# Kernel optimization log

Measured on AMD Instinct MI355X. Metric: run time of the kernel, lower is better.

Reference implementation:

```python
import jax, jax.numpy as jnp
import numpy as np

N, K, F = 65536, 32, 128


def setup_inputs() -> dict:
    key = jax.random.key(0)
    k1, k2, k3, k4 = jax.random.split(key, 4)
    x = jax.random.normal(k1, (N, F), dtype=jnp.float32)
    means = jax.random.normal(k2, (K, F), dtype=jnp.float32)
    # lower-triangular Cholesky factors of precisions with strictly positive diagonal
    a = jax.random.normal(k3, (K, F, F), dtype=jnp.float32) * 0.05
    precisions_chol = jnp.tril(a, k=-1) + jnp.eye(F, dtype=jnp.float32)[None] * (
        1.0 + 0.1 * jax.random.uniform(k3, (K, 1, 1), dtype=jnp.float32)
    )
    # valid mixture weights on the simplex (log is taken in forward)
    u = jax.random.uniform(k4, (K,), dtype=jnp.float32) + 0.1
    weights = u / jnp.sum(u)
    return {"x": x, "means": means, "precisions_chol": precisions_chol, "weights": weights}


def reference(x, means, precisions_chol, weights):
    n_features = x.shape[1]
    # log|prec_chol_k| = sum of log diagonal entries  -> [K]
    log_det = jnp.sum(jnp.log(jnp.diagonal(precisions_chol, axis1=1, axis2=2)), axis=1)
    # whitened residuals: (x - mu_k) @ P_k  done as two batched GEMMs -> [N,K,F]
    y = jnp.einsum("nf,kfg->nkg", x, precisions_chol) - jnp.einsum(
        "kf,kfg->kg", means, precisions_chol
    )[None, :, :]
    log_prob = jnp.sum(y * y, axis=-1)  # Mahalanobis^2, [N,K]
    log2pi = jnp.log(jnp.asarray(2.0 * np.pi, dtype=x.dtype))
    log_gauss = -0.5 * (n_features * log2pi + log_prob) + log_det[None, :]
    # NLL-ish score: logsumexp over components with log mixture weights -> [N]
    return jax.nn.logsumexp(log_gauss + jnp.log(weights)[None, :], axis=1)
```

## Files before the change

### kernel.cpp

```cpp
#include <hip/hip_runtime.h>
#include <hip/hip_bf16.h>


#define NPTS 65536
#define KC 32
#define FD 128
#define SLABB 20480

typedef __attribute__((ext_vector_type(8))) short short8;
typedef __attribute__((ext_vector_type(8))) unsigned short ushort8;
typedef __attribute__((ext_vector_type(16))) float f32x16;

#define MFMA(A, B, C) __builtin_amdgcn_mfma_f32_32x32x16_bf16((A), (B), (C), 0, 0, 0)

static __device__ __forceinline__ unsigned short f2bf(float f) {
  unsigned int u = __float_as_uint(f);
  u += 0x7FFFu + ((u >> 16) & 1u);
  return (unsigned short)(u >> 16);
}

static __device__ __forceinline__ void gll(const unsigned char* g, unsigned char* l) {
  __builtin_amdgcn_global_load_lds((const __attribute__((address_space(1))) void*)g,
                                   (__attribute__((address_space(3))) void*)l, 16, 0, 0);
}

__global__ __launch_bounds__(256) void prep_all(const float* __restrict__ means,
                                                const float* __restrict__ P,
                                                const float* __restrict__ w,
                                                unsigned char* __restrict__ Aimg,
                                                unsigned char* __restrict__ Ximg,
                                                float* __restrict__ ck3) {
  const int k = blockIdx.x;
  const int t = threadIdx.x;
  const float* Pk = P + k * FD * FD;
  __shared__ float Pl[FD * 129];
  __shared__ float smp[FD], r1[FD], r2[FD];
  for (int i = t; i < (FD * FD) / 4; i += 256) {
    const float4 v4 = *(const float4*)(Pk + i * 4);
    const int f = (i * 4) >> 7, c = (i * 4) & 127;
    float* d = Pl + f * 129 + c;
    d[0] = v4.x; d[1] = v4.y; d[2] = v4.z; d[3] = v4.w;
  }
  __syncthreads();
  if (t < FD) {
    float acc = 0.f;
    for (int f = 0; f < FD; ++f) acc = fmaf(means[k * FD + f], Pl[f * 129 + t], acc);
    smp[t] = acc;
    r1[t] = logf(Pl[t * 129 + t]);
    r2[t] = acc * acc;
  }
  __syncthreads();
  if (t < FD) {
    float a2 = 0.f;
    for (int j = 0; j < FD; ++j) a2 = fmaf(Pl[t * 129 + j], smp[j], a2);
    const int id = ((t >> 4) * 64) + k + 32 * ((t >> 3) & 1);
    *(unsigned short*)(Ximg + (size_t)id * 16 + (t & 7) * 2) = f2bf(a2);
  }
  for (int off = 64; off; off >>= 1) {
    if (t < off) { r1[t] += r1[t + off]; r2[t] += r2[t + off]; }
    __syncthreads();
  }
  if (t == 0)
    ck3[k] = logf(w[k]) + r1[0] - 0.5f * ((float)FD * 1.8378770664093453f + r2[0]);
  for (int i = t; i < 1280; i += 256) {
    const int c = i >> 6, l = i & 63;
    int q, s;
    if (c < 8)       { q = 0; s = c; }
    else if (c < 10) { q = 3; s = c - 2; }
    else if (c < 16) { q = 1; s = c - 8; }
    else             { q = 2; s = c - 12; }
    const int g = q * 32 + (l & 31);
    const int f0 = 16 * s + 8 * (l >> 5);
    ushort8 o;
#pragma unroll
    for (int j = 0; j < 8; ++j) o[j] = f2bf(Pl[(f0 + j) * 129 + g]);
    *(ushort8*)(Aimg + (size_t)k * SLABB + (size_t)i * 16) = o;
  }
}

__global__ __launch_bounds__(256, 2) void gmm_main(const float* __restrict__ x,
                                                   const unsigned char* __restrict__ Aimg,
                                                   const unsigned char* __restrict__ Ximg,
                                                   const float* __restrict__ ck3,
                                                   float* __restrict__ out) {
  __shared__ __align__(16) unsigned char abuf[2 * SLABB];
  __shared__ __align__(16) float xvt[4][KC][32];
  __shared__ __align__(16) float xch[2][4][32];
  __shared__ float ck[KC];
  const int tid = threadIdx.x;
  const int wid = tid >> 6;
  const int lane = tid & 63;
  const int half = lane >> 5;
  const int ln = lane & 31;
  const int p = wid & 1;
  const int nq = wid >> 1;
  const int nbase = blockIdx.x * 128;

  if (tid < KC) ck[tid] = ck3[tid];

  {
    const unsigned char* gx = Ximg + wid * 2048 + lane * 16;
    unsigned char* lx = abuf + SLABB + wid * 2048;
    gll(gx, lx);
    gll(gx + 1024, lx + 1024);
    const unsigned char* gs = Aimg + wid * 5120 + lane * 16;
    unsigned char* ls = abuf + wid * 5120;
#pragma unroll
    for (int i = 0; i < 5; ++i) gll(gs + i * 1024, ls + i * 1024);
  }

  short8 xf[2][8];
#pragma unroll
  for (int t = 0; t < 2; ++t) {
    const float* xr = x + (size_t)(nbase + nq * 64 + t * 32 + ln) * FD + 8 * half;
#pragma unroll
    for (int s = 0; s < 8; ++s) {
      const float4 a = *(const float4*)(xr + 16 * s);
      const float4 b = *(const float4*)(xr + 16 * s + 4);
      short8 f;
      f[0] = (short)f2bf(a.x); f[1] = (short)f2bf(a.y);
      f[2] = (short)f2bf(a.z); f[3] = (short)f2bf(a.w);
      f[4] = (short)f2bf(b.x); f[5] = (short)f2bf(b.y);
      f[6] = (short)f2bf(b.z); f[7] = (short)f2bf(b.w);
      xf[t][s] = f;
    }
  }

  f32x16 zc;
#pragma unroll
  for (int i = 0; i < 16; ++i) zc[i] = 0.f;

  asm volatile("s_waitcnt vmcnt(0)" ::: "memory");
  __syncthreads();

  {
    const unsigned char* xb = abuf + SLABB + lane * 16;
    f32x16 xv;
    {
      const short8 fx = *(const short8*)xb;
      xv = MFMA(fx, p ? xf[1][0] : xf[0][0], zc);
    }
#pragma unroll
    for (int s = 1; s < 8; ++s) {
      const short8 fx = *(const short8*)(xb + s * 1024);
      xv = MFMA(fx, p ? xf[1][s] : xf[0][s], xv);
    }
#pragma unroll
    for (int i = 0; i < 16; ++i) {
      const int kk = (i & 3) + 8 * (i >> 2) + 4 * half;
      xvt[wid][kk][ln] = xv[i];
    }
  }
  __syncthreads();

  if (blockIdx.x & 256) {
    __builtin_amdgcn_s_sleep(7);
    __builtin_amdgcn_s_sleep(7);
    __builtin_amdgcn_s_sleep(7);
    __builtin_amdgcn_s_sleep(7);
  }

  float m = -__builtin_inff(), ssum = 0.f;

  for (int k = 0; k < KC; ++k) {
    const int RB = (k & 1) * SLABB;
    const int WB = SLABB - RB;
    const int ph = k & 1;
    const unsigned char* rb = abuf + RB + p * 10240 + lane * 16;
    short8 fr[10];
#pragma unroll
    for (int i = 0; i < 10; ++i) fr[i] = *(const short8*)(rb + i * 1024);
    if (k + 1 < KC) {
      const unsigned char* gs = Aimg + (size_t)(k + 1) * SLABB + wid * 5120 + lane * 16;
      unsigned char* ls = abuf + WB + wid * 5120;
#pragma unroll
      for (int i = 0; i < 5; ++i) gll(gs + i * 1024, ls + i * 1024);
    }
    f32x16 a00, a01, a10, a11;
    __builtin_amdgcn_s_setprio(1);
    if (p == 0) {
      a00 = MFMA(fr[0], xf[0][0], zc);
      a01 = MFMA(fr[0], xf[1][0], zc);
#pragma unroll
      for (int s = 1; s < 8; ++s) {
        a00 = MFMA(fr[s], xf[0][s], a00);
        a01 = MFMA(fr[s], xf[1][s], a01);
      }
      a10 = MFMA(fr[8], xf[0][6], zc);
      a11 = MFMA(fr[8], xf[1][6], zc);
      a10 = MFMA(fr[9], xf[0][7], a10);
      a11 = MFMA(fr[9], xf[1][7], a11);
    } else {
      a00 = MFMA(fr[0], xf[0][2], zc);
      a01 = MFMA(fr[0], xf[1][2], zc);
#pragma unroll
      for (int s = 1; s < 6; ++s) {
        a00 = MFMA(fr[s], xf[0][s + 2], a00);
        a01 = MFMA(fr[s], xf[1][s + 2], a01);
      }
      a10 = MFMA(fr[6], xf[0][4], zc);
      a11 = MFMA(fr[6], xf[1][4], zc);
#pragma unroll
      for (int j = 1; j < 4; ++j) {
        a10 = MFMA(fr[6 + j], xf[0][4 + j], a10);
        a11 = MFMA(fr[6 + j], xf[1][4 + j], a11);
      }
    }
    __builtin_amdgcn_s_setprio(0);
    float q0a = 0.f, q1a = 0.f;
#pragma unroll
    for (int i = 0; i < 16; ++i) {
      q0a = fmaf(a00[i], a00[i], q0a);
      q1a = fmaf(a01[i], a01[i], q1a);
    }
    float q0b = 0.f, q1b = 0.f;
#pragma unroll
    for (int i = 0; i < 16; ++i) {
      q0b = fmaf(a10[i], a10[i], q0b);
      q1b = fmaf(a11[i], a11[i], q1b);
    }
    float q0 = q0a + q0b, q1 = q1a + q1b;
    q0 += __shfl_xor(q0, 32, 64);
    q1 += __shfl_xor(q1, 32, 64);
    float sown = p ? q1 : q0;
    float soth = p ? q0 : q1;
    if (half == 0) xch[ph][wid ^ 1][ln] = soth;
    if (k + 1 < KC) asm volatile("s_waitcnt vmcnt(0)" ::: "memory");
    __syncthreads();
    float sfull = sown + xch[ph][wid][ln];
    sfull = fmaf(-2.f, xvt[wid][k][ln], sfull);
    float vv = ck[k] - 0.5f * sfull;
    float nm = fmaxf(m, vv);
    ssum = ssum * __expf(m - nm) + __expf(vv - nm);
    m = nm;
  }

  if (half == 0) out[nbase + nq * 64 + p * 32 + ln] = m + logf(ssum);
}

extern "C" void kernel_launch(void* const* d_in, const int* in_sizes, int n_in,
                              void* d_out, int out_size, void* d_ws, size_t ws_size,
                              hipStream_t stream) {
  const float* x = (const float*)d_in[0];
  const float* means = (const float*)d_in[1];
  const float* P = (const float*)d_in[2];
  const float* w = (const float*)d_in[3];
  float* out = (float*)d_out;

  unsigned char* ws = (unsigned char*)d_ws;
  unsigned char* Aimg = ws;
  unsigned char* Ximg = ws + 655360;
  float* ck3 = (float*)(ws + 655360 + 8192);

  prep_all<<<32, 256, 0, stream>>>(means, P, w, Aimg, Ximg, ck3);
  gmm_main<<<NPTS / 128, 256, 0, stream>>>(x, Aimg, Ximg, ck3, out);
}
```

Before: 58.27 us.

## Software-pipeline k-loop epilogue behind next component's MFMAs, drop sleep stagger

Restructures the per-component loop so the squared-norm reduction of component k-1 and the logsumexp update of component k-2 are issued before the MFMAs of component k. The aim is to hide the VALU epilogue and the cross-wave exchange latency behind matrix work, and to need one barrier per iteration instead of one after each epilogue. It also removes the s_sleep stagger on half the blocks. The cost is two sets of accumulators held live at once, which raises register pressure at two waves per SIMD.

```diff
diff --git a/kernel.cpp b/kernel.cpp
--- a/kernel.cpp
+++ b/kernel.cpp
@@ -153,19 +153,12 @@
   }
   __syncthreads();
 
-  if (blockIdx.x & 256) {
-    __builtin_amdgcn_s_sleep(7);
-    __builtin_amdgcn_s_sleep(7);
-    __builtin_amdgcn_s_sleep(7);
-    __builtin_amdgcn_s_sleep(7);
-  }
-
-  float m = -__builtin_inff(), ssum = 0.f;
-
-  for (int k = 0; k < KC; ++k) {
+  float m = -__builtin_inff(), ssum = 0.f, sownC = 0.f;
+  f32x16 accA[4], accB[4];
+
+  auto body = [&](int k, f32x16 (&cur)[4], f32x16 (&prev)[4]) {
     const int RB = (k & 1) * SLABB;
     const int WB = SLABB - RB;
-    const int ph = k & 1;
     const unsigned char* rb = abuf + RB + p * 10240 + lane * 16;
     short8 fr[10];
 #pragma unroll
@@ -176,63 +169,97 @@
 #pragma unroll
       for (int i = 0; i < 5; ++i) gll(gs + i * 1024, ls + i * 1024);
     }
-    f32x16 a00, a01, a10, a11;
+    if (k >= 2) {
+      float sfull = sownC + xch[k & 1][wid][ln];
+      sfull = fmaf(-2.f, xvt[wid][k - 2][ln], sfull);
+      float vv = ck[k - 2] - 0.5f * sfull;
+      float nm = fmaxf(m, vv);
+      ssum = ssum * __expf(m - nm) + __expf(vv - nm);
+      m = nm;
+    }
+    if (k >= 1) {
+      float q0a = 0.f, q1a = 0.f, q0b = 0.f, q1b = 0.f;
+#pragma unroll
+      for (int i = 0; i < 16; ++i) {
+        q0a = fmaf(prev[0][i], prev[0][i], q0a);
+        q1a = fmaf(prev[1][i], prev[1][i], q1a);
+        q0b = fmaf(prev[2][i], prev[2][i], q0b);
+        q1b = fmaf(prev[3][i], prev[3][i], q1b);
+      }
+      float q0 = q0a + q0b, q1 = q1a + q1b;
+      q0 += __shfl_xor(q0, 32, 64);
+      q1 += __shfl_xor(q1, 32, 64);
+      sownC = p ? q1 : q0;
+      const float soth = p ? q0 : q1;
+      if (half == 0) xch[(k & 1) ^ 1][wid ^ 1][ln] = soth;
+    }
     __builtin_amdgcn_s_setprio(1);
     if (p == 0) {
-      a00 = MFMA(fr[0], xf[0][0], zc);
-      a01 = MFMA(fr[0], xf[1][0], zc);
+      cur[0] = MFMA(fr[0], xf[0][0], zc);
+      cur[1] = MFMA(fr[0], xf[1][0], zc);
 #pragma unroll
       for (int s = 1; s < 8; ++s) {
-        a00 = MFMA(fr[s], xf[0][s], a00);
-        a01 = MFMA(fr[s], xf[1][s], a01);
-      }
-      a10 = MFMA(fr[8], xf[0][6], zc);
-      a11 = MFMA(fr[8], xf[1][6], zc);
-      a10 = MFMA(fr[9], xf[0][7], a10);
-      a11 = MFMA(fr[9], xf[1][7], a11);
+        cur[0] = MFMA(fr[s], xf[0][s], cur[0]);
+        cur[1] = MFMA(fr[s], xf[1][s], cur[1]);
+      }
+      cur[2] = MFMA(fr[8], xf[0][6], zc);
+      cur[3] = MFMA(fr[8], xf[1][6], zc);
+      cur[2] = MFMA(fr[9], xf[0][7], cur[2]);
+      cur[3] = MFMA(fr[9], xf[1][7], cur[3]);
     } else {
-      a00 = MFMA(fr[0], xf[0][2], zc);
-      a01 = MFMA(fr[0], xf[1][2], zc);
+      cur[0] = MFMA(fr[0], xf[0][2], zc);
+      cur[1] = MFMA(fr[0], xf[1][2], zc);
 #pragma unroll
       for (int s = 1; s < 6; ++s) {
-        a00 = MFMA(fr[s], xf[0][s + 2], a00);
-        a01 = MFMA(fr[s], xf[1][s + 2], a01);
-      }
-      a10 = MFMA(fr[6], xf[0][4], zc);
-      a11 = MFMA(fr[6], xf[1][4], zc);
+        cur[0] = MFMA(fr[s], xf[0][s + 2], cur[0]);
+        cur[1] = MFMA(fr[s], xf[1][s + 2], cur[1]);
+      }
+      cur[2] = MFMA(fr[6], xf[0][4], zc);
+      cur[3] = MFMA(fr[6], xf[1][4], zc);
 #pragma unroll
       for (int j = 1; j < 4; ++j) {
-        a10 = MFMA(fr[6 + j], xf[0][4 + j], a10);
-        a11 = MFMA(fr[6 + j], xf[1][4 + j], a11);
+        cur[2] = MFMA(fr[6 + j], xf[0][4 + j], cur[2]);
+        cur[3] = MFMA(fr[6 + j], xf[1][4 + j], cur[3]);
       }
     }
     __builtin_amdgcn_s_setprio(0);
-    float q0a = 0.f, q1a = 0.f;
+    if (k + 1 < KC) asm volatile("s_waitcnt vmcnt(0)" ::: "memory");
+    __syncthreads();
+  };
+
+  for (int k2 = 0; k2 < KC; k2 += 2) {
+    body(k2, accA, accB);
+    body(k2 + 1, accB, accA);
+  }
+
+  {
+    float sfull = sownC + xch[0][wid][ln];
+    sfull = fmaf(-2.f, xvt[wid][KC - 2][ln], sfull);
+    float vv = ck[KC - 2] - 0.5f * sfull;
+    float nm = fmaxf(m, vv);
+    ssum = ssum * __expf(m - nm) + __expf(vv - nm);
+    m = nm;
+    float q0a = 0.f, q1a = 0.f, q0b = 0.f, q1b = 0.f;
 #pragma unroll
     for (int i = 0; i < 16; ++i) {
-      q0a = fmaf(a00[i], a00[i], q0a);
-      q1a = fmaf(a01[i], a01[i], q1a);
-    }
-    float q0b = 0.f, q1b = 0.f;
-#pragma unroll
-    for (int i = 0; i < 16; ++i) {
-      q0b = fmaf(a10[i], a10[i], q0b);
-      q1b = fmaf(a11[i], a11[i], q1b);
+      q0a = fmaf(accB[0][i], accB[0][i], q0a);
+      q1a = fmaf(accB[1][i], accB[1][i], q1a);
+      q0b = fmaf(accB[2][i], accB[2][i], q0b);
+      q1b = fmaf(accB[3][i], accB[3][i], q1b);
     }
     float q0 = q0a + q0b, q1 = q1a + q1b;
     q0 += __shfl_xor(q0, 32, 64);
     q1 += __shfl_xor(q1, 32, 64);
     float sown = p ? q1 : q0;
-    float soth = p ? q0 : q1;
-    if (half == 0) xch[ph][wid ^ 1][ln] = soth;
-    if (k + 1 < KC) asm volatile("s_waitcnt vmcnt(0)" ::: "memory");
+    const float soth = p ? q0 : q1;
+    if (half == 0) xch[1][wid ^ 1][ln] = soth;
     __syncthreads();
-    float sfull = sown + xch[ph][wid][ln];
-    sfull = fmaf(-2.f, xvt[wid][k][ln], sfull);
-    float vv = ck[k] - 0.5f * sfull;
-    float nm = fmaxf(m, vv);
-    ssum = ssum * __expf(m - nm) + __expf(vv - nm);
-    m = nm;
+    float sf2 = sown + xch[1][wid][ln];
+    sf2 = fmaf(-2.f, xvt[wid][KC - 1][ln], sf2);
+    float v2 = ck[KC - 1] - 0.5f * sf2;
+    float nm2 = fmaxf(m, v2);
+    ssum = ssum * __expf(m - nm2) + __expf(v2 - nm2);
+    m = nm2;
   }
 
   if (half == 0) out[nbase + nq * 64 + p * 32 + ln] = m + logf(ssum);
```

After: 59.92 us. 1.03x slower.
